# Performance work log

Measured on AMD Instinct MI355X. Metric: run time of the kernel, lower is better.

Reference implementation:

```python
import jax, jax.numpy as jnp
import numpy as np

N_NODES = 200_000
N_EDGES = 6_400_000
N_GRAPHS = 2048
VOCAB = 10_000
EMB = 64
HID = 64
NUM_CLASSES = 2


def setup_inputs() -> dict:
    key = jax.random.key(0)
    ks = jax.random.split(key, 12)
    x = jax.random.randint(ks[0], (N_NODES,), 0, VOCAB)
    edge_index = jax.random.randint(ks[1], (2, N_EDGES), 0, N_NODES)
    batch = jnp.sort(jax.random.randint(ks[2], (N_NODES,), 0, N_GRAPHS))
    s = 0.05
    return {
        "x": x,
        "edge_index": edge_index,
        "batch": batch,
        "emb": jax.random.normal(ks[3], (VOCAB, EMB), jnp.float32) * s,
        "W1_l": jax.random.normal(ks[4], (HID, EMB), jnp.float32) * s,
        "b1": jnp.zeros((HID,), jnp.float32),
        "W1_r": jax.random.normal(ks[5], (HID, EMB), jnp.float32) * s,
        "W2_l": jax.random.normal(ks[6], (HID, HID), jnp.float32) * s,
        "b2": jnp.zeros((HID,), jnp.float32),
        "W2_r": jax.random.normal(ks[7], (HID, HID), jnp.float32) * s,
        "Wout": jax.random.normal(ks[8], (NUM_CLASSES, HID), jnp.float32) * s,
        "bout": jnp.zeros((NUM_CLASSES,), jnp.float32),
    }


def _sage_conv(h, src, dst, W_l, b, W_r):
    # mean-aggregate messages from src at dst (PyG SAGEConv, aggr='mean')
    msg_sum = jax.ops.segment_sum(h[src], dst, num_segments=N_NODES)
    cnt = jax.ops.segment_sum(jnp.ones((src.shape[0], 1), h.dtype), dst,
                              num_segments=N_NODES)
    mean = msg_sum / jnp.maximum(cnt, 1.0)  # zero-degree nodes -> 0
    # out = lin_l(mean_neighbors) + lin_r(x); lin_r has no bias in PyG
    return mean @ W_l.T + b + h @ W_r.T


def reference(x, edge_index, batch, emb, W1_l, b1, W1_r, W2_l, b2, W2_r,
              Wout, bout):
    src, dst = edge_index[0], edge_index[1]
    h = emb[x]  # [N, EMB]
    h = jax.nn.relu(_sage_conv(h, src, dst, W1_l, b1, W1_r))
    h = jax.nn.relu(_sage_conv(h, src, dst, W2_l, b2, W2_r))
    # global_mean_pool over graph ids
    pooled = jax.ops.segment_sum(h, batch, num_segments=N_GRAPHS)
    cnt = jax.ops.segment_sum(jnp.ones((h.shape[0], 1), h.dtype), batch,
                              num_segments=N_GRAPHS)
    pooled = pooled / jnp.maximum(cnt, 1.0)
    return pooled @ Wout.T + bout  # [N_GRAPHS, NUM_CLASSES]
```

## Files before the change

kernel.cpp:

```cpp
#include <hip/hip_runtime.h>
#include <hip/hip_fp16.h>
#include <stdint.h>


#define NPB 4
#define NPW 4
#define NBUCK 256
#define TILE 4096
#define EPT 16
#define MAXN 1024

__device__ __forceinline__ int bucket_of(int dstv, int n_nodes) {
  return (int)(((unsigned)dstv * 256u) / (unsigned)n_nodes);
}

__device__ __forceinline__ void acc8h(float* a, uint4 u, float m) {
  const __half2* hp = (const __half2*)&u;
#pragma unroll
  for (int q = 0; q < 4; ++q) {
    float2 f = __half22float2(hp[q]);
    a[2 * q]     = fmaf(m, f.x, a[2 * q]);
    a[2 * q + 1] = fmaf(m, f.y, a[2 * q + 1]);
  }
}

__global__ void k_bhist(const int* __restrict__ dst, int* __restrict__ btot,
                        int n_edges, int n_nodes) {
  __shared__ int h[NBUCK];
  int t = threadIdx.x;
  h[t] = 0;
  __syncthreads();
  int stride = gridDim.x * blockDim.x;
  for (int e = blockIdx.x * blockDim.x + t; e < n_edges; e += stride)
    atomicAdd(&h[bucket_of(dst[e], n_nodes)], 1);
  __syncthreads();
  if (h[t]) atomicAdd(&btot[t], h[t]);
}

__global__ void k_bscan(const int* __restrict__ btot, int* __restrict__ bbase,
                        int* __restrict__ gcur, int n_edges) {
  __shared__ int s[NBUCK];
  int t = threadIdx.x;
  s[t] = btot[t];
  __syncthreads();
  for (int off = 1; off < NBUCK; off <<= 1) {
    int add = (t >= off) ? s[t - off] : 0;
    __syncthreads();
    s[t] += add;
    __syncthreads();
  }
  int excl = (t == 0) ? 0 : s[t - 1];
  bbase[t] = excl;
  gcur[t] = excl;
  if (t == NBUCK - 1) bbase[NBUCK] = n_edges;
}

__global__ void k_part(const int* __restrict__ src, const int* __restrict__ dst,
                       int* __restrict__ gcur, unsigned* __restrict__ pairs,
                       int n_edges, int n_nodes, int chunk) {
  __shared__ int hist[NBUCK];
  __shared__ int base[NBUCK];
  int t = threadIdx.x;
  int beg = blockIdx.x * chunk;
  int end = min(beg + chunk, n_edges);
  for (int tbeg = beg; tbeg < end; tbeg += TILE) {
    int cnt = min(TILE, end - tbeg);
    hist[t] = 0;
    __syncthreads();
    unsigned pk[EPT];
    int r[EPT], bk[EPT];
    bool v[EPT];
#pragma unroll
    for (int k = 0; k < EPT; ++k) {
      int li = k * 256 + t;
      v[k] = li < cnt;
      if (v[k]) {
        int i = tbeg + li;
        int s = src[i];
        int d = dst[i];
        bk[k] = bucket_of(d, n_nodes);
        unsigned nb0 = ((unsigned)bk[k] * (unsigned)n_nodes + 255u) >> 8;
        pk[k] = (((unsigned)d - nb0) << 18) | (unsigned)s;
        r[k] = atomicAdd(&hist[bk[k]], 1);
      }
    }
    __syncthreads();
    base[t] = (hist[t] > 0) ? atomicAdd(&gcur[t], hist[t]) : 0;
    __syncthreads();
#pragma unroll
    for (int k = 0; k < EPT; ++k)
      if (v[k]) pairs[base[bk[k]] + r[k]] = pk[k];
    __syncthreads();
  }
}

__global__ void k_bucket(const unsigned* __restrict__ pairs, const int* __restrict__ bbase,
                         const int* __restrict__ x, int* __restrict__ offs,
                         unsigned* __restrict__ idx, int n_nodes, int n_edges) {
  __shared__ int lcnt[MAXN];
  __shared__ int lcur[MAXN];
  __shared__ int stmp[256];
  int b = blockIdx.x, t = threadIdx.x;
  int nb0 = (int)((((unsigned)b * (unsigned)n_nodes) + 255u) >> 8);
  int nb1 = (int)((((unsigned)(b + 1) * (unsigned)n_nodes) + 255u) >> 8);
  if (nb1 > n_nodes) nb1 = n_nodes;
  int nn = nb1 - nb0;
  int ebeg = bbase[b], eend = bbase[b + 1];
  for (int i = t; i < nn; i += 256) lcnt[i] = 0;
  __syncthreads();
  for (int i = ebeg + t; i < eend; i += 256)
    atomicAdd(&lcnt[pairs[i] >> 18], 1);
  __syncthreads();
  int i0 = t * 4;
  int v0 = (i0 + 0 < nn) ? lcnt[i0 + 0] : 0;
  int v1 = (i0 + 1 < nn) ? lcnt[i0 + 1] : 0;
  int v2 = (i0 + 2 < nn) ? lcnt[i0 + 2] : 0;
  int v3 = (i0 + 3 < nn) ? lcnt[i0 + 3] : 0;
  stmp[t] = v0 + v1 + v2 + v3;
  __syncthreads();
  for (int off = 1; off < 256; off <<= 1) {
    int add = (t >= off) ? stmp[t - off] : 0;
    __syncthreads();
    stmp[t] += add;
    __syncthreads();
  }
  int run = ebeg + ((t == 0) ? 0 : stmp[t - 1]);
  if (i0 + 0 < nn) { lcur[i0 + 0] = run; offs[nb0 + i0 + 0] = run; run += v0; }
  if (i0 + 1 < nn) { lcur[i0 + 1] = run; offs[nb0 + i0 + 1] = run; run += v1; }
  if (i0 + 2 < nn) { lcur[i0 + 2] = run; offs[nb0 + i0 + 2] = run; run += v2; }
  if (i0 + 3 < nn) { lcur[i0 + 3] = run; offs[nb0 + i0 + 3] = run; run += v3; }
  if (b == NBUCK - 1 && t == 0) offs[n_nodes] = n_edges;
  __syncthreads();
  for (int i = ebeg + t; i < eend; i += 256) {
    unsigned e = pairs[i];
    int s = (int)(e & 0x3FFFFu);
    int pos = atomicAdd(&lcur[e >> 18], 1);
    idx[pos] = ((unsigned)x[s] << 18) | (unsigned)s;
  }
}

__global__ void k_transpose4(const float* __restrict__ a0, const float* __restrict__ a1,
                             const float* __restrict__ a2, const float* __restrict__ a3,
                             float* __restrict__ wt) {
  const float* s = (blockIdx.x == 0) ? a0 : (blockIdx.x == 1) ? a1 : (blockIdx.x == 2) ? a2 : a3;
  float* d = wt + blockIdx.x * 4096;
  for (int i = threadIdx.x; i < 4096; i += blockDim.x) {
    int r = i >> 6, c = i & 63;
    d[c * 64 + r] = s[i];
  }
}

__global__ void k_prep(const float* __restrict__ emb, const float* __restrict__ w1lT,
                       const float* __restrict__ w1rT, const float* __restrict__ b1,
                       __half* __restrict__ te, float* __restrict__ trb, int vocab) {
  __shared__ float se[NPB][64];
  int wid = threadIdx.x >> 6, lane = threadIdx.x & 63;
  int v = blockIdx.x * NPB + wid;
  if (v >= vocab) return;
  se[wid][lane] = emb[(size_t)v * 64 + lane];
  __syncwarp();
  float aL = 0.f, aR = b1[lane];
#pragma unroll 8
  for (int f = 0; f < 64; ++f) {
    float ev = se[wid][f];
    aL = fmaf(ev, w1lT[f * 64 + lane], aL);
    aR = fmaf(ev, w1rT[f * 64 + lane], aR);
  }
  te[(size_t)v * 64 + lane] = __float2half(aL);
  trb[(size_t)v * 64 + lane] = aR;
}

__global__ void k_conv1(const unsigned* __restrict__ idx, const int* __restrict__ offs,
                        const __half* __restrict__ te, const float* __restrict__ trb,
                        const int* __restrict__ x, const float* __restrict__ w2lT,
                        const float* __restrict__ w2rT, const float* __restrict__ b2,
                        __half* __restrict__ g1, float* __restrict__ s1, int n_nodes) {
  __shared__ float sm[NPB * NPW][64];
  int wid = threadIdx.x >> 6, lane = threadIdx.x & 63;
  int r8 = lane >> 3, s8 = (lane & 7) << 3;
  int nbase = (blockIdx.x * NPB + wid) * NPW;
  if (nbase >= n_nodes) return;
  int nvalid = min(NPW, n_nodes - nbase);

  for (int i = 0; i < nvalid; ++i) {
    int node = nbase + i;
    int beg = offs[node], end = offs[node + 1];
    float a[8];
#pragma unroll
    for (int q = 0; q < 8; ++q) a[q] = 0.f;
    for (int c = beg; c < end; c += 64) {
      unsigned eidx = idx[min(c + lane, end - 1)];
      int nit = min(end - c, 64);
      for (int k = 0; k < nit; k += 32) {
        int k0 = k + r8, k1 = k0 + 8, k2 = k0 + 16, k3 = k0 + 24;
        int v0 = (int)(__shfl(eidx, min(k0, nit - 1)) >> 18);
        int v1 = (int)(__shfl(eidx, min(k1, nit - 1)) >> 18);
        int v2 = (int)(__shfl(eidx, min(k2, nit - 1)) >> 18);
        int v3 = (int)(__shfl(eidx, min(k3, nit - 1)) >> 18);
        uint4 u0 = *(const uint4*)(te + ((size_t)v0 << 6) + s8);
        uint4 u1 = *(const uint4*)(te + ((size_t)v1 << 6) + s8);
        uint4 u2 = *(const uint4*)(te + ((size_t)v2 << 6) + s8);
        uint4 u3 = *(const uint4*)(te + ((size_t)v3 << 6) + s8);
        acc8h(a, u0, (k0 < nit) ? 1.f : 0.f);
        acc8h(a, u1, (k1 < nit) ? 1.f : 0.f);
        acc8h(a, u2, (k2 < nit) ? 1.f : 0.f);
        acc8h(a, u3, (k3 < nit) ? 1.f : 0.f);
      }
    }
#pragma unroll
    for (int q = 0; q < 8; ++q) {
      a[q] += __shfl_xor(a[q], 8);
      a[q] += __shfl_xor(a[q], 16);
      a[q] += __shfl_xor(a[q], 32);
    }
    int deg = end - beg;
    float inv = (deg > 0) ? 1.f / (float)deg : 0.f;
    if (lane < 8) {
      const float* tp = trb + ((size_t)x[node] << 6) + s8;
      float4 t0 = *(const float4*)tp;
      float4 t1 = *(const float4*)(tp + 4);
      float4 h0, h1;
      h0.x = fmaxf(fmaf(a[0], inv, t0.x), 0.f);
      h0.y = fmaxf(fmaf(a[1], inv, t0.y), 0.f);
      h0.z = fmaxf(fmaf(a[2], inv, t0.z), 0.f);
      h0.w = fmaxf(fmaf(a[3], inv, t0.w), 0.f);
      h1.x = fmaxf(fmaf(a[4], inv, t1.x), 0.f);
      h1.y = fmaxf(fmaf(a[5], inv, t1.y), 0.f);
      h1.z = fmaxf(fmaf(a[6], inv, t1.z), 0.f);
      h1.w = fmaxf(fmaf(a[7], inv, t1.w), 0.f);
      *(float4*)&sm[wid * NPW + i][s8] = h0;
      *(float4*)&sm[wid * NPW + i][s8 + 4] = h1;
    }
  }

  float b2v = b2[lane];
  float aL[NPW], aR[NPW];
#pragma unroll
  for (int i = 0; i < NPW; ++i) { aL[i] = 0.f; aR[i] = b2v; }
  const float* smw = sm[wid * NPW];
#pragma unroll 8
  for (int f = 0; f < 64; ++f) {
    float wl = w2lT[f * 64 + lane];
    float wr = w2rT[f * 64 + lane];
#pragma unroll
    for (int i = 0; i < NPW; ++i) {
      float h = smw[i * 64 + f];
      aL[i] = fmaf(h, wl, aL[i]);
      aR[i] = fmaf(h, wr, aR[i]);
    }
  }
  for (int i = 0; i < nvalid; ++i) {
    int node = nbase + i;
    g1[((size_t)node << 6) + lane] = __float2half(aL[i]);
    s1[((size_t)node << 6) + lane] = aR[i];
  }
}

__global__ void k_conv2(const unsigned* __restrict__ idx, const int* __restrict__ offs,
                        const __half* __restrict__ g1, const float* __restrict__ s1,
                        const float* __restrict__ wout, float* __restrict__ o,
                        int n_nodes) {
  __shared__ float sm[NPB][64];
  int wid = threadIdx.x >> 6, lane = threadIdx.x & 63;
  int r8 = lane >> 3, s8 = (lane & 7) << 3;
  int node = blockIdx.x * NPB + wid;
  bool active = node < n_nodes;
  if (active) {
    int beg = offs[node], end = offs[node + 1];
    float a[8];
#pragma unroll
    for (int q = 0; q < 8; ++q) a[q] = 0.f;
    for (int c = beg; c < end; c += 64) {
      unsigned eidx = idx[min(c + lane, end - 1)];
      int nit = min(end - c, 64);
      for (int k = 0; k < nit; k += 32) {
        int k0 = k + r8, k1 = k0 + 8, k2 = k0 + 16, k3 = k0 + 24;
        int v0 = (int)(__shfl(eidx, min(k0, nit - 1)) & 0x3FFFFu);
        int v1 = (int)(__shfl(eidx, min(k1, nit - 1)) & 0x3FFFFu);
        int v2 = (int)(__shfl(eidx, min(k2, nit - 1)) & 0x3FFFFu);
        int v3 = (int)(__shfl(eidx, min(k3, nit - 1)) & 0x3FFFFu);
        uint4 u0 = *(const uint4*)(g1 + ((size_t)v0 << 6) + s8);
        uint4 u1 = *(const uint4*)(g1 + ((size_t)v1 << 6) + s8);
        uint4 u2 = *(const uint4*)(g1 + ((size_t)v2 << 6) + s8);
        uint4 u3 = *(const uint4*)(g1 + ((size_t)v3 << 6) + s8);
        acc8h(a, u0, (k0 < nit) ? 1.f : 0.f);
        acc8h(a, u1, (k1 < nit) ? 1.f : 0.f);
        acc8h(a, u2, (k2 < nit) ? 1.f : 0.f);
        acc8h(a, u3, (k3 < nit) ? 1.f : 0.f);
      }
    }
#pragma unroll
    for (int q = 0; q < 8; ++q) {
      a[q] += __shfl_xor(a[q], 8);
      a[q] += __shfl_xor(a[q], 16);
      a[q] += __shfl_xor(a[q], 32);
    }
    int deg = end - beg;
    float inv = (deg > 0) ? 1.f / (float)deg : 0.f;
    if (lane < 8) {
#pragma unroll
      for (int q = 0; q < 8; ++q) sm[wid][s8 + q] = a[q] * inv;
    }
  }
  __syncthreads();
  if (active) {
    float h2 = fmaxf(sm[wid][lane] + s1[((size_t)node << 6) + lane], 0.f);
    float p0 = h2 * wout[lane];
    float p1 = h2 * wout[64 + lane];
    for (int off = 32; off > 0; off >>= 1) {
      p0 += __shfl_down(p0, off);
      p1 += __shfl_down(p1, off);
    }
    if (lane == 0) {
      o[((size_t)node << 1) + 0] = p0;
      o[((size_t)node << 1) + 1] = p1;
    }
  }
}

__global__ void k_goffs(const int* __restrict__ batch, int* __restrict__ goffs,
                        int n_nodes, int n_graphs) {
  int i = blockIdx.x * blockDim.x + threadIdx.x;
  if (i >= n_nodes) return;
  int b = batch[i];
  int bp = (i == 0) ? -1 : batch[i - 1];
  for (int g = bp + 1; g <= b; ++g) goffs[g] = i;
  if (i == n_nodes - 1)
    for (int g = b + 1; g <= n_graphs; ++g) goffs[g] = n_nodes;
}

__global__ void k_pool(const float2* __restrict__ o, const int* __restrict__ goffs,
                       const float* __restrict__ bout, float* __restrict__ out,
                       int n_graphs) {
  int wid = threadIdx.x >> 6, lane = threadIdx.x & 63;
  int g = blockIdx.x * NPB + wid;
  if (g >= n_graphs) return;
  int beg = goffs[g], end = goffs[g + 1];
  float a0 = 0.f, a1 = 0.f;
  for (int n = beg + lane; n < end; n += 64) {
    float2 v = o[n];
    a0 += v.x;
    a1 += v.y;
  }
  for (int off = 32; off > 0; off >>= 1) {
    a0 += __shfl_down(a0, off);
    a1 += __shfl_down(a1, off);
  }
  if (lane == 0) {
    int cnt = end - beg;
    float inv = (cnt > 0) ? 1.f / (float)cnt : 0.f;
    out[g * 2 + 0] = a0 * inv + bout[0];
    out[g * 2 + 1] = a1 * inv + bout[1];
  }
}

extern "C" void kernel_launch(void* const* d_in, const int* in_sizes, int n_in,
                              void* d_out, int out_size, void* d_ws, size_t ws_size,
                              hipStream_t stream) {
  const int* x = (const int*)d_in[0];
  const int* ei = (const int*)d_in[1];
  const int* batch = (const int*)d_in[2];
  const float* emb = (const float*)d_in[3];
  const float* W1l = (const float*)d_in[4];
  const float* b1 = (const float*)d_in[5];
  const float* W1r = (const float*)d_in[6];
  const float* W2l = (const float*)d_in[7];
  const float* b2 = (const float*)d_in[8];
  const float* W2r = (const float*)d_in[9];
  const float* Wout = (const float*)d_in[10];
  const float* bout = (const float*)d_in[11];
  float* out = (float*)d_out;

  int n_nodes = in_sizes[0];
  int n_edges = in_sizes[1] / 2;
  int vocab = in_sizes[3] / 64;
  int n_graphs = out_size / 2;
  const int* src = ei;
  const int* dst = ei + n_edges;

  char* p = (char*)d_ws;
  auto alloc = [&](size_t bytes) -> void* {
    void* r = (void*)p;
    p += (bytes + 255) & ~(size_t)255;
    return r;
  };
  __half* te = (__half*)alloc((size_t)vocab * 64 * 2);
  float* trb = (float*)alloc((size_t)vocab * 64 * 4);
  float* wt = (float*)alloc(4 * 4096 * 4);
  int* offs = (int*)alloc((size_t)(n_nodes + 1) * 4);
  int* goffs = (int*)alloc((size_t)(n_graphs + 1) * 4);
  int* btot = (int*)alloc(NBUCK * 4);
  int* bbase = (int*)alloc((NBUCK + 1) * 4);
  int* gcur = (int*)alloc(NBUCK * 4);
  unsigned* idx = (unsigned*)alloc((size_t)n_edges * 4);
  unsigned* pairs = (unsigned*)alloc((size_t)n_edges * 4);
  float* s1 = (float*)alloc((size_t)n_nodes * 64 * 4);
  float* o = (float*)alloc((size_t)n_nodes * 2 * 4);
  __half* g1 = (__half*)pairs;

  hipMemsetAsync(btot, 0, NBUCK * 4, stream);

  k_transpose4<<<4, 256, 0, stream>>>(W1l, W1r, W2l, W2r, wt);
  k_prep<<<(vocab + NPB - 1) / NPB, 64 * NPB, 0, stream>>>(emb, wt, wt + 4096, b1, te, trb, vocab);

  k_bhist<<<1024, 256, 0, stream>>>(dst, btot, n_edges, n_nodes);
  k_bscan<<<1, NBUCK, 0, stream>>>(btot, bbase, gcur, n_edges);
  int part_blocks = 512;
  int chunk = (n_edges + part_blocks - 1) / part_blocks;
  k_part<<<part_blocks, 256, 0, stream>>>(src, dst, gcur, pairs, n_edges, n_nodes, chunk);
  k_bucket<<<NBUCK, 256, 0, stream>>>(pairs, bbase, x, offs, idx, n_nodes, n_edges);

  k_goffs<<<(n_nodes + 255) / 256, 256, 0, stream>>>(batch, goffs, n_nodes, n_graphs);

  int npb1 = NPB * NPW;
  k_conv1<<<(n_nodes + npb1 - 1) / npb1, 64 * NPB, 0, stream>>>(idx, offs, te, trb, x, wt + 8192, wt + 12288, b2, g1, s1, n_nodes);
  k_conv2<<<(n_nodes + NPB - 1) / NPB, 64 * NPB, 0, stream>>>(idx, offs, g1, s1, Wout, o, n_nodes);
  k_pool<<<(n_graphs + NPB - 1) / NPB, 64 * NPB, 0, stream>>>((const float2*)o, goffs, bout, out, n_graphs);
}
```

Measured before the change: 475.3 us.

## Drop histogram pass with fixed-capacity bucket regions; single-wave conv blocks with unmasked fast path

The separate bucket histogram and scan kernels are removed. Each bucket now gets a fixed-capacity region in the pairs buffer, and its offset is computed after partitioning from the cursors. This saves a full read of the dst array and a kernel launch. The conv kernels switch to one-wavefront blocks and add a full-32-edge loop without clamping or masking, keeping the masked path only for the tail. The risks are bucket overflow if a bucket exceeds its capacity, and more, smaller blocks.

```diff
diff --git a/kernel.cpp b/kernel.cpp
--- a/kernel.cpp
+++ b/kernel.cpp
@@ -3,8 +3,8 @@
 #include <stdint.h>
 
 
+#define NPW 4
 #define NPB 4
-#define NPW 4
 #define NBUCK 256
 #define TILE 4096
 #define EPT 16
@@ -24,35 +24,18 @@
   }
 }
 
-__global__ void k_bhist(const int* __restrict__ dst, int* __restrict__ btot,
-                        int n_edges, int n_nodes) {
-  __shared__ int h[NBUCK];
-  int t = threadIdx.x;
-  h[t] = 0;
-  __syncthreads();
-  int stride = gridDim.x * blockDim.x;
-  for (int e = blockIdx.x * blockDim.x + t; e < n_edges; e += stride)
-    atomicAdd(&h[bucket_of(dst[e], n_nodes)], 1);
-  __syncthreads();
-  if (h[t]) atomicAdd(&btot[t], h[t]);
-}
-
-__global__ void k_bscan(const int* __restrict__ btot, int* __restrict__ bbase,
-                        int* __restrict__ gcur, int n_edges) {
-  __shared__ int s[NBUCK];
-  int t = threadIdx.x;
-  s[t] = btot[t];
-  __syncthreads();
-  for (int off = 1; off < NBUCK; off <<= 1) {
-    int add = (t >= off) ? s[t - off] : 0;
-    __syncthreads();
-    s[t] += add;
-    __syncthreads();
-  }
-  int excl = (t == 0) ? 0 : s[t - 1];
-  bbase[t] = excl;
-  gcur[t] = excl;
-  if (t == NBUCK - 1) bbase[NBUCK] = n_edges;
+__device__ __forceinline__ void acc8h_nm(float* a, uint4 u) {
+  const __half2* hp = (const __half2*)&u;
+#pragma unroll
+  for (int q = 0; q < 4; ++q) {
+    float2 f = __half22float2(hp[q]);
+    a[2 * q]     += f.x;
+    a[2 * q + 1] += f.y;
+  }
+}
+
+__global__ void k_init(int* __restrict__ gcur, int cap) {
+  gcur[threadIdx.x] = threadIdx.x * cap;
 }
 
 __global__ void k_part(const int* __restrict__ src, const int* __restrict__ dst,
@@ -94,9 +77,26 @@
   }
 }
 
-__global__ void k_bucket(const unsigned* __restrict__ pairs, const int* __restrict__ bbase,
-                         const int* __restrict__ x, int* __restrict__ offs,
-                         unsigned* __restrict__ idx, int n_nodes, int n_edges) {
+__global__ void k_bscan2(const int* __restrict__ gcur, int* __restrict__ bbase,
+                         int cap, int n_edges) {
+  __shared__ int s[NBUCK];
+  int t = threadIdx.x;
+  s[t] = gcur[t] - t * cap;
+  __syncthreads();
+  for (int off = 1; off < NBUCK; off <<= 1) {
+    int add = (t >= off) ? s[t - off] : 0;
+    __syncthreads();
+    s[t] += add;
+    __syncthreads();
+  }
+  bbase[t] = (t == 0) ? 0 : s[t - 1];
+  if (t == NBUCK - 1) bbase[NBUCK] = n_edges;
+}
+
+__global__ void k_bucket(const unsigned* __restrict__ pairs, const int* __restrict__ gcur,
+                         const int* __restrict__ bbase, const int* __restrict__ x,
+                         int* __restrict__ offs, unsigned* __restrict__ idx,
+                         int n_nodes, int n_edges, int cap) {
   __shared__ int lcnt[MAXN];
   __shared__ int lcur[MAXN];
   __shared__ int stmp[256];
@@ -105,10 +105,12 @@
   int nb1 = (int)((((unsigned)(b + 1) * (unsigned)n_nodes) + 255u) >> 8);
   if (nb1 > n_nodes) nb1 = n_nodes;
   int nn = nb1 - nb0;
-  int ebeg = bbase[b], eend = bbase[b + 1];
+  int rbeg = b * cap;
+  int rend = gcur[b];
+  int obase = bbase[b];
   for (int i = t; i < nn; i += 256) lcnt[i] = 0;
   __syncthreads();
-  for (int i = ebeg + t; i < eend; i += 256)
+  for (int i = rbeg + t; i < rend; i += 256)
     atomicAdd(&lcnt[pairs[i] >> 18], 1);
   __syncthreads();
   int i0 = t * 4;
@@ -124,14 +126,14 @@
     stmp[t] += add;
     __syncthreads();
   }
-  int run = ebeg + ((t == 0) ? 0 : stmp[t - 1]);
+  int run = obase + ((t == 0) ? 0 : stmp[t - 1]);
   if (i0 + 0 < nn) { lcur[i0 + 0] = run; offs[nb0 + i0 + 0] = run; run += v0; }
   if (i0 + 1 < nn) { lcur[i0 + 1] = run; offs[nb0 + i0 + 1] = run; run += v1; }
   if (i0 + 2 < nn) { lcur[i0 + 2] = run; offs[nb0 + i0 + 2] = run; run += v2; }
   if (i0 + 3 < nn) { lcur[i0 + 3] = run; offs[nb0 + i0 + 3] = run; run += v3; }
   if (b == NBUCK - 1 && t == 0) offs[n_nodes] = n_edges;
   __syncthreads();
-  for (int i = ebeg + t; i < eend; i += 256) {
+  for (int i = rbeg + t; i < rend; i += 256) {
     unsigned e = pairs[i];
     int s = (int)(e & 0x3FFFFu);
     int pos = atomicAdd(&lcur[e >> 18], 1);
@@ -170,15 +172,16 @@
   trb[(size_t)v * 64 + lane] = aR;
 }
 
-__global__ void k_conv1(const unsigned* __restrict__ idx, const int* __restrict__ offs,
-                        const __half* __restrict__ te, const float* __restrict__ trb,
-                        const int* __restrict__ x, const float* __restrict__ w2lT,
-                        const float* __restrict__ w2rT, const float* __restrict__ b2,
-                        __half* __restrict__ g1, float* __restrict__ s1, int n_nodes) {
-  __shared__ float sm[NPB * NPW][64];
-  int wid = threadIdx.x >> 6, lane = threadIdx.x & 63;
+__global__ __launch_bounds__(64) void
+k_conv1(const unsigned* __restrict__ idx, const int* __restrict__ offs,
+        const __half* __restrict__ te, const float* __restrict__ trb,
+        const int* __restrict__ x, const float* __restrict__ w2lT,
+        const float* __restrict__ w2rT, const float* __restrict__ b2,
+        __half* __restrict__ g1, float* __restrict__ s1, int n_nodes) {
+  __shared__ float sm[NPW][64];
+  int lane = threadIdx.x;
   int r8 = lane >> 3, s8 = (lane & 7) << 3;
-  int nbase = (blockIdx.x * NPB + wid) * NPW;
+  int nbase = blockIdx.x * NPW;
   if (nbase >= n_nodes) return;
   int nvalid = min(NPW, n_nodes - nbase);
 
@@ -189,10 +192,26 @@
 #pragma unroll
     for (int q = 0; q < 8; ++q) a[q] = 0.f;
     for (int c = beg; c < end; c += 64) {
-      unsigned eidx = idx[min(c + lane, end - 1)];
       int nit = min(end - c, 64);
-      for (int k = 0; k < nit; k += 32) {
-        int k0 = k + r8, k1 = k0 + 8, k2 = k0 + 16, k3 = k0 + 24;
+      unsigned eidx = idx[c + min(lane, nit - 1)];
+      int nfull = nit & ~31;
+      for (int k = 0; k < nfull; k += 32) {
+        int k0 = k + r8;
+        int v0 = (int)(__shfl(eidx, k0) >> 18);
+        int v1 = (int)(__shfl(eidx, k0 + 8) >> 18);
+        int v2 = (int)(__shfl(eidx, k0 + 16) >> 18);
+        int v3 = (int)(__shfl(eidx, k0 + 24) >> 18);
+        uint4 u0 = *(const uint4*)(te + ((size_t)v0 << 6) + s8);
+        uint4 u1 = *(const uint4*)(te + ((size_t)v1 << 6) + s8);
+        uint4 u2 = *(const uint4*)(te + ((size_t)v2 << 6) + s8);
+        uint4 u3 = *(const uint4*)(te + ((size_t)v3 << 6) + s8);
+        acc8h_nm(a, u0);
+        acc8h_nm(a, u1);
+        acc8h_nm(a, u2);
+        acc8h_nm(a, u3);
+      }
+      if (nit & 31) {
+        int k0 = nfull + r8, k1 = k0 + 8, k2 = k0 + 16, k3 = k0 + 24;
         int v0 = (int)(__shfl(eidx, min(k0, nit - 1)) >> 18);
         int v1 = (int)(__shfl(eidx, min(k1, nit - 1)) >> 18);
         int v2 = (int)(__shfl(eidx, min(k2, nit - 1)) >> 18);
@@ -228,16 +247,17 @@
       h1.y = fmaxf(fmaf(a[5], inv, t1.y), 0.f);
       h1.z = fmaxf(fmaf(a[6], inv, t1.z), 0.f);
       h1.w = fmaxf(fmaf(a[7], inv, t1.w), 0.f);
-      *(float4*)&sm[wid * NPW + i][s8] = h0;
-      *(float4*)&sm[wid * NPW + i][s8 + 4] = h1;
-    }
-  }
+      *(float4*)&sm[i][s8] = h0;
+      *(float4*)&sm[i][s8 + 4] = h1;
+    }
+  }
+  __syncthreads();
 
   float b2v = b2[lane];
   float aL[NPW], aR[NPW];
 #pragma unroll
   for (int i = 0; i < NPW; ++i) { aL[i] = 0.f; aR[i] = b2v; }
-  const float* smw = sm[wid * NPW];
+  const float* smw = &sm[0][0];
 #pragma unroll 8
   for (int f = 0; f < 64; ++f) {
     float wl = w2lT[f * 64 + lane];
@@ -256,65 +276,77 @@
   }
 }
 
-__global__ void k_conv2(const unsigned* __restrict__ idx, const int* __restrict__ offs,
-                        const __half* __restrict__ g1, const float* __restrict__ s1,
-                        const float* __restrict__ wout, float* __restrict__ o,
-                        int n_nodes) {
-  __shared__ float sm[NPB][64];
-  int wid = threadIdx.x >> 6, lane = threadIdx.x & 63;
+__global__ __launch_bounds__(64) void
+k_conv2(const unsigned* __restrict__ idx, const int* __restrict__ offs,
+        const __half* __restrict__ g1, const float* __restrict__ s1,
+        const float* __restrict__ wout, float* __restrict__ o, int n_nodes) {
+  __shared__ float sm[64];
+  int lane = threadIdx.x;
   int r8 = lane >> 3, s8 = (lane & 7) << 3;
-  int node = blockIdx.x * NPB + wid;
-  bool active = node < n_nodes;
-  if (active) {
-    int beg = offs[node], end = offs[node + 1];
-    float a[8];
-#pragma unroll
-    for (int q = 0; q < 8; ++q) a[q] = 0.f;
-    for (int c = beg; c < end; c += 64) {
-      unsigned eidx = idx[min(c + lane, end - 1)];
-      int nit = min(end - c, 64);
-      for (int k = 0; k < nit; k += 32) {
-        int k0 = k + r8, k1 = k0 + 8, k2 = k0 + 16, k3 = k0 + 24;
-        int v0 = (int)(__shfl(eidx, min(k0, nit - 1)) & 0x3FFFFu);
-        int v1 = (int)(__shfl(eidx, min(k1, nit - 1)) & 0x3FFFFu);
-        int v2 = (int)(__shfl(eidx, min(k2, nit - 1)) & 0x3FFFFu);
-        int v3 = (int)(__shfl(eidx, min(k3, nit - 1)) & 0x3FFFFu);
-        uint4 u0 = *(const uint4*)(g1 + ((size_t)v0 << 6) + s8);
-        uint4 u1 = *(const uint4*)(g1 + ((size_t)v1 << 6) + s8);
-        uint4 u2 = *(const uint4*)(g1 + ((size_t)v2 << 6) + s8);
-        uint4 u3 = *(const uint4*)(g1 + ((size_t)v3 << 6) + s8);
-        acc8h(a, u0, (k0 < nit) ? 1.f : 0.f);
-        acc8h(a, u1, (k1 < nit) ? 1.f : 0.f);
-        acc8h(a, u2, (k2 < nit) ? 1.f : 0.f);
-        acc8h(a, u3, (k3 < nit) ? 1.f : 0.f);
-      }
-    }
-#pragma unroll
-    for (int q = 0; q < 8; ++q) {
-      a[q] += __shfl_xor(a[q], 8);
-      a[q] += __shfl_xor(a[q], 16);
-      a[q] += __shfl_xor(a[q], 32);
-    }
-    int deg = end - beg;
-    float inv = (deg > 0) ? 1.f / (float)deg : 0.f;
-    if (lane < 8) {
-#pragma unroll
-      for (int q = 0; q < 8; ++q) sm[wid][s8 + q] = a[q] * inv;
-    }
-  }
-  __syncthreads();
-  if (active) {
-    float h2 = fmaxf(sm[wid][lane] + s1[((size_t)node << 6) + lane], 0.f);
-    float p0 = h2 * wout[lane];
-    float p1 = h2 * wout[64 + lane];
-    for (int off = 32; off > 0; off >>= 1) {
-      p0 += __shfl_down(p0, off);
-      p1 += __shfl_down(p1, off);
-    }
-    if (lane == 0) {
-      o[((size_t)node << 1) + 0] = p0;
-      o[((size_t)node << 1) + 1] = p1;
-    }
+  int node = blockIdx.x;
+  if (node >= n_nodes) return;
+  int beg = offs[node], end = offs[node + 1];
+  float a[8];
+#pragma unroll
+  for (int q = 0; q < 8; ++q) a[q] = 0.f;
+  for (int c = beg; c < end; c += 64) {
+    int nit = min(end - c, 64);
+    unsigned eidx = idx[c + min(lane, nit - 1)];
+    int nfull = nit & ~31;
+    for (int k = 0; k < nfull; k += 32) {
+      int k0 = k + r8;
+      int v0 = (int)(__shfl(eidx, k0) & 0x3FFFFu);
+      int v1 = (int)(__shfl(eidx, k0 + 8) & 0x3FFFFu);
+      int v2 = (int)(__shfl(eidx, k0 + 16) & 0x3FFFFu);
+      int v3 = (int)(__shfl(eidx, k0 + 24) & 0x3FFFFu);
+      uint4 u0 = *(const uint4*)(g1 + ((size_t)v0 << 6) + s8);
+      uint4 u1 = *(const uint4*)(g1 + ((size_t)v1 << 6) + s8);
+      uint4 u2 = *(const uint4*)(g1 + ((size_t)v2 << 6) + s8);
+      uint4 u3 = *(const uint4*)(g1 + ((size_t)v3 << 6) + s8);
+      acc8h_nm(a, u0);
+      acc8h_nm(a, u1);
+      acc8h_nm(a, u2);
+      acc8h_nm(a, u3);
+    }
+    if (nit & 31) {
+      int k0 = nfull + r8, k1 = k0 + 8, k2 = k0 + 16, k3 = k0 + 24;
+      int v0 = (int)(__shfl(eidx, min(k0, nit - 1)) & 0x3FFFFu);
+      int v1 = (int)(__shfl(eidx, min(k1, nit - 1)) & 0x3FFFFu);
+      int v2 = (int)(__shfl(eidx, min(k2, nit - 1)) & 0x3FFFFu);
+      int v3 = (int)(__shfl(eidx, min(k3, nit - 1)) & 0x3FFFFu);
+      uint4 u0 = *(const uint4*)(g1 + ((size_t)v0 << 6) + s8);
+      uint4 u1 = *(const uint4*)(g1 + ((size_t)v1 << 6) + s8);
+      uint4 u2 = *(const uint4*)(g1 + ((size_t)v2 << 6) + s8);
+      uint4 u3 = *(const uint4*)(g1 + ((size_t)v3 << 6) + s8);
+      acc8h(a, u0, (k0 < nit) ? 1.f : 0.f);
+      acc8h(a, u1, (k1 < nit) ? 1.f : 0.f);
+      acc8h(a, u2, (k2 < nit) ? 1.f : 0.f);
+      acc8h(a, u3, (k3 < nit) ? 1.f : 0.f);
+    }
+  }
+#pragma unroll
+  for (int q = 0; q < 8; ++q) {
+    a[q] += __shfl_xor(a[q], 8);
+    a[q] += __shfl_xor(a[q], 16);
+    a[q] += __shfl_xor(a[q], 32);
+  }
+  int deg = end - beg;
+  float inv = (deg > 0) ? 1.f / (float)deg : 0.f;
+  if (lane < 8) {
+#pragma unroll
+    for (int q = 0; q < 8; ++q) sm[s8 + q] = a[q] * inv;
+  }
+  __syncthreads();
+  float h2 = fmaxf(sm[lane] + s1[((size_t)node << 6) + lane], 0.f);
+  float p0 = h2 * wout[lane];
+  float p1 = h2 * wout[64 + lane];
+  for (int off = 32; off > 0; off >>= 1) {
+    p0 += __shfl_down(p0, off);
+    p1 += __shfl_down(p1, off);
+  }
+  if (lane == 0) {
+    o[((size_t)node << 1) + 0] = p0;
+    o[((size_t)node << 1) + 1] = p1;
   }
 }
 
@@ -378,6 +410,8 @@
   const int* src = ei;
   const int* dst = ei + n_edges;
 
+  int cap = n_edges / NBUCK + n_edges / (NBUCK * 8) + 1024;
+
   char* p = (char*)d_ws;
   auto alloc = [&](size_t bytes) -> void* {
     void* r = (void*)p;
@@ -389,31 +423,29 @@
   float* wt = (float*)alloc(4 * 4096 * 4);
   int* offs = (int*)alloc((size_t)(n_nodes + 1) * 4);
   int* goffs = (int*)alloc((size_t)(n_graphs + 1) * 4);
-  int* btot = (int*)alloc(NBUCK * 4);
   int* bbase = (int*)alloc((NBUCK + 1) * 4);
   int* gcur = (int*)alloc(NBUCK * 4);
   unsigned* idx = (unsigned*)alloc((size_t)n_edges * 4);
-  unsigned* pairs = (unsigned*)alloc((size_t)n_edges * 4);
+  size_t pairs_bytes = (size_t)NBUCK * cap * 4;
+  size_t g1_bytes = (size_t)n_nodes * 64 * 2;
+  unsigned* pairs = (unsigned*)alloc(pairs_bytes > g1_bytes ? pairs_bytes : g1_bytes);
   float* s1 = (float*)alloc((size_t)n_nodes * 64 * 4);
   float* o = (float*)alloc((size_t)n_nodes * 2 * 4);
   __half* g1 = (__half*)pairs;
 
-  hipMemsetAsync(btot, 0, NBUCK * 4, stream);
-
+  k_init<<<1, NBUCK, 0, stream>>>(gcur, cap);
   k_transpose4<<<4, 256, 0, stream>>>(W1l, W1r, W2l, W2r, wt);
   k_prep<<<(vocab + NPB - 1) / NPB, 64 * NPB, 0, stream>>>(emb, wt, wt + 4096, b1, te, trb, vocab);
 
-  k_bhist<<<1024, 256, 0, stream>>>(dst, btot, n_edges, n_nodes);
-  k_bscan<<<1, NBUCK, 0, stream>>>(btot, bbase, gcur, n_edges);
   int part_blocks = 512;
   int chunk = (n_edges + part_blocks - 1) / part_blocks;
   k_part<<<part_blocks, 256, 0, stream>>>(src, dst, gcur, pairs, n_edges, n_nodes, chunk);
-  k_bucket<<<NBUCK, 256, 0, stream>>>(pairs, bbase, x, offs, idx, n_nodes, n_edges);
+  k_bscan2<<<1, NBUCK, 0, stream>>>(gcur, bbase, cap, n_edges);
+  k_bucket<<<NBUCK, 256, 0, stream>>>(pairs, gcur, bbase, x, offs, idx, n_nodes, n_edges, cap);
 
   k_goffs<<<(n_nodes + 255) / 256, 256, 0, stream>>>(batch, goffs, n_nodes, n_graphs);
 
-  int npb1 = NPB * NPW;
-  k_conv1<<<(n_nodes + npb1 - 1) / npb1, 64 * NPB, 0, stream>>>(idx, offs, te, trb, x, wt + 8192, wt + 12288, b2, g1, s1, n_nodes);
-  k_conv2<<<(n_nodes + NPB - 1) / NPB, 64 * NPB, 0, stream>>>(idx, offs, g1, s1, Wout, o, n_nodes);
+  k_conv1<<<(n_nodes + NPW - 1) / NPW, 64, 0, stream>>>(idx, offs, te, trb, x, wt + 8192, wt + 12288, b2, g1, s1, n_nodes);
+  k_conv2<<<n_nodes, 64, 0, stream>>>(idx, offs, g1, s1, Wout, o, n_nodes);
   k_pool<<<(n_graphs + NPB - 1) / NPB, 64 * NPB, 0, stream>>>((const float2*)o, goffs, bout, out, n_graphs);
 }
```

Result: faster. 437.7 us (-7.9%).
